# Kernel tuning notes

Hardware: AMD Instinct MI355X
Metric: run time of the kernel (lower is better)

Reference implementation:

```python
import jax, jax.numpy as jnp
import numpy as np

N_NODES = 50000
N_EDGES = 800000
IN_CH = 14     # x has 2 pos cols + 14 feature cols
HID = 16
N_REGIONS = 10


def _init_linear(key, fan_in, fan_out):
    k1, k2 = jax.random.split(key)
    bound = 1.0 / np.sqrt(fan_in)
    W = jax.random.uniform(k1, (fan_in, fan_out), minval=-bound, maxval=bound, dtype=jnp.float32)
    b = jax.random.uniform(k2, (fan_out,), minval=-bound, maxval=bound, dtype=jnp.float32)
    return W, b


def setup_inputs() -> dict:
    key = jax.random.key(0)
    ks = jax.random.split(key, 16)
    x = jax.random.normal(ks[0], (N_NODES, 2 + IN_CH), dtype=jnp.float32)
    edge_index = jax.random.randint(ks[1], (2, N_EDGES), 0, N_NODES, dtype=jnp.int64)
    node_region = jax.random.randint(ks[2], (N_NODES,), 0, N_REGIONS, dtype=jnp.int64)

    inp = {"x": x, "edge_index": edge_index, "node_region": node_region}
    # 3 RSGCN layers: lin_in maps coors(2) -> in_c*hidden, lin_out maps hidden -> hidden
    in_chs = [IN_CH, HID, HID]
    for li, ic in enumerate(in_chs, start=1):
        Wi, bi = _init_linear(ks[2 + 2 * li], 2, ic * HID)
        Wo, bo = _init_linear(ks[3 + 2 * li], HID, HID)
        inp[f"W_in{li}"] = Wi; inp[f"b_in{li}"] = bi
        inp[f"W_out{li}"] = Wo; inp[f"b_out{li}"] = bo
    # decoder
    inp["Wd1"], inp["bd1"] = _init_linear(ks[10], 2 * HID, HID)
    inp["Wd2"], inp["bd2"] = _init_linear(ks[11], HID, HID)
    inp["Wd3"], inp["bd3"] = _init_linear(ks[12], HID, 1)
    return inp


def _rsgcn_layer(h, pos, src, dst, same_region, W_in, b_in, W_out, b_out):
    # Spatial graph conv (SGCN-style) with region-specific gating.
    E = src.shape[0]
    in_c = h.shape[1]
    rel = pos[dst] - pos[src]                                   # [E, 2]
    spatial = jax.nn.relu(rel @ W_in + b_in).reshape(E, in_c, HID)  # [E, in_c, hid]
    msg = jnp.einsum('ec,ech->eh', h[src], spatial)             # [E, hid]
    msg = msg * same_region                                     # region-specific gate
    agg = jax.ops.segment_sum(msg, dst, num_segments=N_NODES)   # [N, hid]
    cnt = jax.ops.segment_sum(jnp.ones((E,), h.dtype), dst, num_segments=N_NODES)
    agg = agg / jnp.maximum(cnt, 1.0)[:, None]                  # mean aggregation
    return jax.nn.relu(agg @ W_out + b_out)                     # dropout is identity in eval


def reference(x, edge_index, node_region,
              W_in1, b_in1, W_out1, b_out1,
              W_in2, b_in2, W_out2, b_out2,
              W_in3, b_in3, W_out3, b_out3,
              Wd1, bd1, Wd2, bd2, Wd3, bd3):
    pos = x[:, :2]
    h = x[:, 2:]
    src, dst = edge_index[0], edge_index[1]
    same = (node_region[src] == node_region[dst]).astype(x.dtype)[:, None]
    h = _rsgcn_layer(h, pos, src, dst, same, W_in1, b_in1, W_out1, b_out1)
    h = _rsgcn_layer(h, pos, src, dst, same, W_in2, b_in2, W_out2, b_out2)
    h = _rsgcn_layer(h, pos, src, dst, same, W_in3, b_in3, W_out3, b_out3)
    # decoder: per-edge link score
    z = jnp.concatenate([h[src], h[dst]], axis=-1)              # [E, 2*hid]
    z = jax.nn.relu(z @ Wd1 + bd1)
    z = jax.nn.relu(z @ Wd2 + bd2)
    return jax.nn.sigmoid(z @ Wd3 + bd3)                        # [E, 1]
```

## Files before the change

### kernel.cpp

```cpp
#include <hip/hip_runtime.h>
#include <math.h>

#define N_NODES 50000
#define N_EDGES 800000
#define HID 16
#define SCAN_BLOCKS ((N_NODES + 255) / 256)

__global__ void count_kernel(const int* __restrict__ src,
                             const int* __restrict__ dst,
                             const int* __restrict__ region,
                             int* __restrict__ cnt_all,
                             int* __restrict__ cnt_act) {
    int e = blockIdx.x * blockDim.x + threadIdx.x;
    int s = src[e];
    int d = dst[e];
    atomicAdd(cnt_all + d, 1);
    if (region[s] == region[d]) atomicAdd(cnt_act + d, 1);
}

__global__ void scanA_kernel(const int* __restrict__ cnt_act,
                             int* __restrict__ blockSums) {
    __shared__ int red[256];
    int i = blockIdx.x * 256 + threadIdx.x;
    red[threadIdx.x] = (i < N_NODES) ? cnt_act[i] : 0;
    __syncthreads();
    for (int off = 128; off > 0; off >>= 1) {
        if (threadIdx.x < off) red[threadIdx.x] += red[threadIdx.x + off];
        __syncthreads();
    }
    if (threadIdx.x == 0) blockSums[blockIdx.x] = red[0];
}

__global__ void scanB_kernel(const int* __restrict__ blockSums,
                             int* __restrict__ blockOff) {
    __shared__ int s[256];
    int t = threadIdx.x;
    s[t] = (t < SCAN_BLOCKS) ? blockSums[t] : 0;
    __syncthreads();
    for (int off = 1; off < 256; off <<= 1) {
        int v = (t >= off) ? s[t - off] : 0;
        __syncthreads();
        s[t] += v;
        __syncthreads();
    }
    if (t < SCAN_BLOCKS) blockOff[t] = (t == 0) ? 0 : s[t - 1];
}

__global__ void scanC_kernel(const int* __restrict__ cnt_act,
                             const int* __restrict__ blockOff,
                             int* __restrict__ row_ptr) {
    __shared__ int s[256];
    int t = threadIdx.x;
    int i = blockIdx.x * 256 + t;
    int v = (i < N_NODES) ? cnt_act[i] : 0;
    s[t] = v;
    __syncthreads();
    for (int off = 1; off < 256; off <<= 1) {
        int u = (t >= off) ? s[t - off] : 0;
        __syncthreads();
        s[t] += u;
        __syncthreads();
    }
    if (i < N_NODES) row_ptr[i] = blockOff[blockIdx.x] + s[t] - v;
}

__global__ void fill_kernel(const int* __restrict__ src,
                            const int* __restrict__ dst,
                            const int* __restrict__ region,
                            const int* __restrict__ row_ptr,
                            int* __restrict__ cursor,
                            int* __restrict__ csr_eid) {
    int e = blockIdx.x * blockDim.x + threadIdx.x;
    int s = src[e];
    int d = dst[e];
    if (region[s] == region[d]) {
        int pos = row_ptr[d] + atomicAdd(cursor + d, 1);
        csr_eid[pos] = e;
    }
}

template <int IN_C>
__global__ void layer_gather(const float* __restrict__ x,
                             const float* __restrict__ hbase,
                             const int* __restrict__ src,
                             const int* __restrict__ csr_eid,
                             const int* __restrict__ row_ptr,
                             const int* __restrict__ cnt_act,
                             const int* __restrict__ cnt_all,
                             const float* __restrict__ Win,
                             const float* __restrict__ bin,
                             const float* __restrict__ Wout,
                             const float* __restrict__ bout,
                             float* __restrict__ hout) {
    int t = blockIdx.x * blockDim.x + threadIdx.x;
    int n = t >> 4;
    int j = t & 15;

    float w0[IN_C], w1[IN_C], bb[IN_C];
#pragma unroll
    for (int c = 0; c < IN_C; ++c) {
        w0[c] = Win[c * HID + j];
        w1[c] = Win[IN_C * HID + c * HID + j];
        bb[c] = bin[c * HID + j];
    }

    float px = x[n * 16 + 0];
    float py = x[n * 16 + 1];

    int beg = row_ptr[n];
    int cntA = cnt_act[n];

    float msg = 0.0f;
    for (int k = 0; k < cntA; ++k) {
        int e = csr_eid[beg + k];
        int s = src[e];
        float rx = px - x[s * 16 + 0];
        float ry = py - x[s * 16 + 1];
        const float* hs = hbase + s * 16;
        float m = 0.0f;
#pragma unroll
        for (int c = 0; c < IN_C; ++c) {
            float sp = fmaf(rx, w0[c], fmaf(ry, w1[c], bb[c]));
            sp = fmaxf(sp, 0.0f);
            m = fmaf(hs[c], sp, m);
        }
        msg += m;
    }

    float inv = 1.0f / fmaxf((float)cnt_all[n], 1.0f);
    float a = msg * inv;

    int lane_base = (threadIdx.x & 63) & 0x30;
    float o = bout[j];
#pragma unroll
    for (int c = 0; c < HID; ++c) {
        float ac = __shfl(a, lane_base + c, 64);
        o = fmaf(ac, Wout[c * HID + j], o);
    }
    hout[n * HID + j] = fmaxf(o, 0.0f);
}

__global__ void decoder_kernel(const float* __restrict__ h,
                               const int* __restrict__ src,
                               const int* __restrict__ dst,
                               const float* __restrict__ Wd1,
                               const float* __restrict__ bd1,
                               const float* __restrict__ Wd2,
                               const float* __restrict__ bd2,
                               const float* __restrict__ Wd3,
                               const float* __restrict__ bd3,
                               float* __restrict__ out) {
    int e = blockIdx.x * blockDim.x + threadIdx.x;
    if (e >= N_EDGES) return;
    int s = src[e];
    int d = dst[e];

    float z[32];
    const float4* hs = (const float4*)(h + s * HID);
    const float4* hd = (const float4*)(h + d * HID);
#pragma unroll
    for (int q = 0; q < 4; ++q) {
        float4 v = hs[q];
        z[q * 4 + 0] = v.x; z[q * 4 + 1] = v.y; z[q * 4 + 2] = v.z; z[q * 4 + 3] = v.w;
    }
#pragma unroll
    for (int q = 0; q < 4; ++q) {
        float4 v = hd[q];
        z[16 + q * 4 + 0] = v.x; z[16 + q * 4 + 1] = v.y; z[16 + q * 4 + 2] = v.z; z[16 + q * 4 + 3] = v.w;
    }

    float d1[HID];
#pragma unroll
    for (int j = 0; j < HID; ++j) d1[j] = bd1[j];
#pragma unroll
    for (int c = 0; c < 32; ++c) {
        float zc = z[c];
#pragma unroll
        for (int j = 0; j < HID; ++j) d1[j] = fmaf(zc, Wd1[c * HID + j], d1[j]);
    }
#pragma unroll
    for (int j = 0; j < HID; ++j) d1[j] = fmaxf(d1[j], 0.0f);

    float d2[HID];
#pragma unroll
    for (int j = 0; j < HID; ++j) d2[j] = bd2[j];
#pragma unroll
    for (int c = 0; c < HID; ++c) {
        float dc = d1[c];
#pragma unroll
        for (int j = 0; j < HID; ++j) d2[j] = fmaf(dc, Wd2[c * HID + j], d2[j]);
    }

    float o = bd3[0];
#pragma unroll
    for (int j = 0; j < HID; ++j) o = fmaf(fmaxf(d2[j], 0.0f), Wd3[j], o);

    out[e] = 1.0f / (1.0f + __expf(-o));
}

extern "C" void kernel_launch(void* const* d_in, const int* in_sizes, int n_in,
                              void* d_out, int out_size, void* d_ws, size_t ws_size,
                              hipStream_t stream) {
    const float* x      = (const float*)d_in[0];
    const int*   edge   = (const int*)d_in[1];
    const int*   region = (const int*)d_in[2];
    const float* W_in1  = (const float*)d_in[3];
    const float* b_in1  = (const float*)d_in[4];
    const float* W_out1 = (const float*)d_in[5];
    const float* b_out1 = (const float*)d_in[6];
    const float* W_in2  = (const float*)d_in[7];
    const float* b_in2  = (const float*)d_in[8];
    const float* W_out2 = (const float*)d_in[9];
    const float* b_out2 = (const float*)d_in[10];
    const float* W_in3  = (const float*)d_in[11];
    const float* b_in3  = (const float*)d_in[12];
    const float* W_out3 = (const float*)d_in[13];
    const float* b_out3 = (const float*)d_in[14];
    const float* Wd1    = (const float*)d_in[15];
    const float* bd1    = (const float*)d_in[16];
    const float* Wd2    = (const float*)d_in[17];
    const float* bd2    = (const float*)d_in[18];
    const float* Wd3    = (const float*)d_in[19];
    const float* bd3    = (const float*)d_in[20];
    float* out = (float*)d_out;

    const int* src = edge;
    const int* dst = edge + N_EDGES;

    float* ws        = (float*)d_ws;
    float* hA        = ws;
    float* hB        = hA + N_NODES * HID;
    int*   cnt_all   = (int*)(hB + N_NODES * HID);
    int*   cnt_act   = cnt_all + N_NODES;
    int*   row_ptr   = cnt_act + N_NODES;
    int*   cursor    = row_ptr + N_NODES;
    int*   blockSums = cursor + N_NODES;
    int*   blockOff  = blockSums + 256;
    int*   csr_eid   = (int*)d_out;

    const int BLK = 256;
    const int egrid = N_EDGES / BLK;
    const int lgrid = N_NODES * HID / BLK;

    hipMemsetAsync(cnt_all, 0, (size_t)(4 * N_NODES) * sizeof(int), stream);

    count_kernel<<<egrid, BLK, 0, stream>>>(src, dst, region, cnt_all, cnt_act);
    scanA_kernel<<<SCAN_BLOCKS, 256, 0, stream>>>(cnt_act, blockSums);
    scanB_kernel<<<1, 256, 0, stream>>>(blockSums, blockOff);
    scanC_kernel<<<SCAN_BLOCKS, 256, 0, stream>>>(cnt_act, blockOff, row_ptr);
    fill_kernel<<<egrid, BLK, 0, stream>>>(src, dst, region, row_ptr, cursor, csr_eid);

    layer_gather<14><<<lgrid, BLK, 0, stream>>>(x, x + 2, src, csr_eid, row_ptr,
                                                cnt_act, cnt_all, W_in1, b_in1,
                                                W_out1, b_out1, hA);
    layer_gather<16><<<lgrid, BLK, 0, stream>>>(x, hA, src, csr_eid, row_ptr,
                                                cnt_act, cnt_all, W_in2, b_in2,
                                                W_out2, b_out2, hB);
    layer_gather<16><<<lgrid, BLK, 0, stream>>>(x, hB, src, csr_eid, row_ptr,
                                                cnt_act, cnt_all, W_in3, b_in3,
                                                W_out3, b_out3, hA);

    decoder_kernel<<<egrid, BLK, 0, stream>>>(hA, src, dst, Wd1, bd1, Wd2, bd2, Wd3, bd3, out);
}
```

Baseline: 242.0 us.

## Precompute per-node decoder first-layer projections and process four edges per thread

The first decoder linear layer is split into per-node halves. The last GCN layer now computes u = h·Wd1_top and v = h·Wd1_bottom once per node, so the per-edge work becomes an add of u[src] and v[dst] instead of a 32x16 matmul. The decoder also handles four edges per thread, using vectorized int4 index loads, shared Wd2 row loads and a float4 output store. This trades a larger per-node buffer (32 floats per node) and higher register pressure for far fewer per-edge FLOPs.

```diff
diff --git a/kernel.cpp b/kernel.cpp
--- a/kernel.cpp
+++ b/kernel.cpp
@@ -5,6 +5,7 @@
 #define N_EDGES 800000
 #define HID 16
 #define SCAN_BLOCKS ((N_NODES + 255) / 256)
+#define EPT 4
 
 __global__ void count_kernel(const int* __restrict__ src,
                              const int* __restrict__ dst,
@@ -79,7 +80,7 @@
     }
 }
 
-template <int IN_C>
+template <int IN_C, bool WRITE_UV>
 __global__ void layer_gather(const float* __restrict__ x,
                              const float* __restrict__ hbase,
                              const int* __restrict__ src,
@@ -91,6 +92,7 @@
                              const float* __restrict__ bin,
                              const float* __restrict__ Wout,
                              const float* __restrict__ bout,
+                             const float* __restrict__ Wd1,
                              float* __restrict__ hout) {
     int t = blockIdx.x * blockDim.x + threadIdx.x;
     int n = t >> 4;
@@ -137,65 +139,115 @@
         float ac = __shfl(a, lane_base + c, 64);
         o = fmaf(ac, Wout[c * HID + j], o);
     }
-    hout[n * HID + j] = fmaxf(o, 0.0f);
-}
-
-__global__ void decoder_kernel(const float* __restrict__ h,
+    float hval = fmaxf(o, 0.0f);
+
+    if (!WRITE_UV) {
+        hout[n * HID + j] = hval;
+    } else {
+        float u = 0.0f, v = 0.0f;
+#pragma unroll
+        for (int c = 0; c < HID; ++c) {
+            float hc = __shfl(hval, lane_base + c, 64);
+            u = fmaf(hc, Wd1[c * HID + j], u);
+            v = fmaf(hc, Wd1[(HID + c) * HID + j], v);
+        }
+        hout[n * 32 + j]       = u;
+        hout[n * 32 + 16 + j]  = v;
+    }
+}
+
+__global__ void decoder_kernel(const float* __restrict__ uv,
                                const int* __restrict__ src,
                                const int* __restrict__ dst,
-                               const float* __restrict__ Wd1,
                                const float* __restrict__ bd1,
                                const float* __restrict__ Wd2,
                                const float* __restrict__ bd2,
                                const float* __restrict__ Wd3,
                                const float* __restrict__ bd3,
                                float* __restrict__ out) {
-    int e = blockIdx.x * blockDim.x + threadIdx.x;
-    if (e >= N_EDGES) return;
-    int s = src[e];
-    int d = dst[e];
-
-    float z[32];
-    const float4* hs = (const float4*)(h + s * HID);
-    const float4* hd = (const float4*)(h + d * HID);
+    int i = blockIdx.x * blockDim.x + threadIdx.x;
+    if (i * EPT >= N_EDGES) return;
+
+    const int4* src4 = (const int4*)src;
+    const int4* dst4 = (const int4*)dst;
+    int4 s4 = src4[i];
+    int4 d4 = dst4[i];
+    int ss[EPT] = {s4.x, s4.y, s4.z, s4.w};
+    int dd[EPT] = {d4.x, d4.y, d4.z, d4.w};
+
+    float b1[HID];
+    const float4* b1p = (const float4*)bd1;
 #pragma unroll
     for (int q = 0; q < 4; ++q) {
-        float4 v = hs[q];
-        z[q * 4 + 0] = v.x; z[q * 4 + 1] = v.y; z[q * 4 + 2] = v.z; z[q * 4 + 3] = v.w;
-    }
+        float4 b = b1p[q];
+        b1[q*4+0] = b.x; b1[q*4+1] = b.y; b1[q*4+2] = b.z; b1[q*4+3] = b.w;
+    }
+
+    float d1[EPT][HID];
+#pragma unroll
+    for (int e = 0; e < EPT; ++e) {
+        const float4* us = (const float4*)(uv + (size_t)ss[e] * 32);
+        const float4* vd = (const float4*)(uv + (size_t)dd[e] * 32 + 16);
+#pragma unroll
+        for (int q = 0; q < 4; ++q) {
+            float4 a = us[q];
+            float4 b = vd[q];
+            d1[e][q*4+0] = fmaxf(a.x + b.x + b1[q*4+0], 0.0f);
+            d1[e][q*4+1] = fmaxf(a.y + b.y + b1[q*4+1], 0.0f);
+            d1[e][q*4+2] = fmaxf(a.z + b.z + b1[q*4+2], 0.0f);
+            d1[e][q*4+3] = fmaxf(a.w + b.w + b1[q*4+3], 0.0f);
+        }
+    }
+
+    float acc[EPT][HID];
+    const float4* b2p = (const float4*)bd2;
 #pragma unroll
     for (int q = 0; q < 4; ++q) {
-        float4 v = hd[q];
-        z[16 + q * 4 + 0] = v.x; z[16 + q * 4 + 1] = v.y; z[16 + q * 4 + 2] = v.z; z[16 + q * 4 + 3] = v.w;
-    }
-
-    float d1[HID];
-#pragma unroll
-    for (int j = 0; j < HID; ++j) d1[j] = bd1[j];
-#pragma unroll
-    for (int c = 0; c < 32; ++c) {
-        float zc = z[c];
-#pragma unroll
-        for (int j = 0; j < HID; ++j) d1[j] = fmaf(zc, Wd1[c * HID + j], d1[j]);
-    }
-#pragma unroll
-    for (int j = 0; j < HID; ++j) d1[j] = fmaxf(d1[j], 0.0f);
-
-    float d2[HID];
-#pragma unroll
-    for (int j = 0; j < HID; ++j) d2[j] = bd2[j];
+        float4 b = b2p[q];
+#pragma unroll
+        for (int e = 0; e < EPT; ++e) {
+            acc[e][q*4+0] = b.x; acc[e][q*4+1] = b.y;
+            acc[e][q*4+2] = b.z; acc[e][q*4+3] = b.w;
+        }
+    }
+
 #pragma unroll
     for (int c = 0; c < HID; ++c) {
-        float dc = d1[c];
-#pragma unroll
-        for (int j = 0; j < HID; ++j) d2[j] = fmaf(dc, Wd2[c * HID + j], d2[j]);
-    }
-
-    float o = bd3[0];
-#pragma unroll
-    for (int j = 0; j < HID; ++j) o = fmaf(fmaxf(d2[j], 0.0f), Wd3[j], o);
-
-    out[e] = 1.0f / (1.0f + __expf(-o));
+        const float4* wr = (const float4*)(Wd2 + c * HID);
+        float w[HID];
+#pragma unroll
+        for (int q = 0; q < 4; ++q) {
+            float4 wv = wr[q];
+            w[q*4+0] = wv.x; w[q*4+1] = wv.y; w[q*4+2] = wv.z; w[q*4+3] = wv.w;
+        }
+#pragma unroll
+        for (int e = 0; e < EPT; ++e) {
+            float dc = d1[e][c];
+#pragma unroll
+            for (int j = 0; j < HID; ++j) acc[e][j] = fmaf(dc, w[j], acc[e][j]);
+        }
+    }
+
+    float w3[HID];
+    const float4* w3p = (const float4*)Wd3;
+#pragma unroll
+    for (int q = 0; q < 4; ++q) {
+        float4 wv = w3p[q];
+        w3[q*4+0] = wv.x; w3[q*4+1] = wv.y; w3[q*4+2] = wv.z; w3[q*4+3] = wv.w;
+    }
+    float b3 = bd3[0];
+
+    float4 res;
+    float r[EPT];
+#pragma unroll
+    for (int e = 0; e < EPT; ++e) {
+        float o = b3;
+#pragma unroll
+        for (int j = 0; j < HID; ++j) o = fmaf(fmaxf(acc[e][j], 0.0f), w3[j], o);
+        r[e] = 1.0f / (1.0f + __expf(-o));
+    }
+    res.x = r[0]; res.y = r[1]; res.z = r[2]; res.w = r[3];
+    ((float4*)out)[i] = res;
 }
 
 extern "C" void kernel_launch(void* const* d_in, const int* in_sizes, int n_in,
@@ -230,7 +282,8 @@
     float* ws        = (float*)d_ws;
     float* hA        = ws;
     float* hB        = hA + N_NODES * HID;
-    int*   cnt_all   = (int*)(hB + N_NODES * HID);
+    float* uv        = hB + N_NODES * HID;
+    int*   cnt_all   = (int*)(uv + N_NODES * 32);
     int*   cnt_act   = cnt_all + N_NODES;
     int*   row_ptr   = cnt_act + N_NODES;
     int*   cursor    = row_ptr + N_NODES;
@@ -241,6 +294,7 @@
     const int BLK = 256;
     const int egrid = N_EDGES / BLK;
     const int lgrid = N_NODES * HID / BLK;
+    const int dgrid = (N_EDGES / EPT + BLK - 1) / BLK;
 
     hipMemsetAsync(cnt_all, 0, (size_t)(4 * N_NODES) * sizeof(int), stream);
 
@@ -250,15 +304,15 @@
     scanC_kernel<<<SCAN_BLOCKS, 256, 0, stream>>>(cnt_act, blockOff, row_ptr);
     fill_kernel<<<egrid, BLK, 0, stream>>>(src, dst, region, row_ptr, cursor, csr_eid);
 
-    layer_gather<14><<<lgrid, BLK, 0, stream>>>(x, x + 2, src, csr_eid, row_ptr,
-                                                cnt_act, cnt_all, W_in1, b_in1,
-                                                W_out1, b_out1, hA);
-    layer_gather<16><<<lgrid, BLK, 0, stream>>>(x, hA, src, csr_eid, row_ptr,
-                                                cnt_act, cnt_all, W_in2, b_in2,
-                                                W_out2, b_out2, hB);
-    layer_gather<16><<<lgrid, BLK, 0, stream>>>(x, hB, src, csr_eid, row_ptr,
-                                                cnt_act, cnt_all, W_in3, b_in3,
-                                                W_out3, b_out3, hA);
-
-    decoder_kernel<<<egrid, BLK, 0, stream>>>(hA, src, dst, Wd1, bd1, Wd2, bd2, Wd3, bd3, out);
-}
+    layer_gather<14, false><<<lgrid, BLK, 0, stream>>>(x, x + 2, src, csr_eid, row_ptr,
+                                                       cnt_act, cnt_all, W_in1, b_in1,
+                                                       W_out1, b_out1, nullptr, hA);
+    layer_gather<16, false><<<lgrid, BLK, 0, stream>>>(x, hA, src, csr_eid, row_ptr,
+                                                       cnt_act, cnt_all, W_in2, b_in2,
+                                                       W_out2, b_out2, nullptr, hB);
+    layer_gather<16, true><<<lgrid, BLK, 0, stream>>>(x, hB, src, csr_eid, row_ptr,
+                                                      cnt_act, cnt_all, W_in3, b_in3,
+                                                      W_out3, b_out3, Wd1, uv);
+
+    decoder_kernel<<<dgrid, BLK, 0, stream>>>(uv, src, dst, bd1, Wd2, bd2, Wd3, bd3, out);
+}
```

New measurement: 257.7 us. 1.07x slower.

## Precompute per-edge CSR records with source id and relative position

Applied to the files above, without the earlier changes.

The fill kernel now writes a packed float4 record per active edge (source index plus precomputed relative position) into CSR order. This removes the csr_eid->src->x indirection chain in all three gather layers. The block-offset scan and row-pointer scan are merged into one kernel that also seeds the cursor and computes inverse degree, which drops a kernel launch and a memset region. The decoder is reordered to use fewer live registers. The cost is extra workspace for the records and extra writes in the fill pass.

```diff
diff --git a/kernel.cpp b/kernel.cpp
--- a/kernel.cpp
+++ b/kernel.cpp
@@ -5,13 +5,14 @@
 #define N_EDGES 800000
 #define HID 16
 #define SCAN_BLOCKS ((N_NODES + 255) / 256)
+#define BLK 256
 
 __global__ void count_kernel(const int* __restrict__ src,
                              const int* __restrict__ dst,
                              const int* __restrict__ region,
                              int* __restrict__ cnt_all,
                              int* __restrict__ cnt_act) {
-    int e = blockIdx.x * blockDim.x + threadIdx.x;
+    int e = blockIdx.x * BLK + threadIdx.x;
     int s = src[e];
     int d = dst[e];
     atomicAdd(cnt_all + d, 1);
@@ -20,79 +21,90 @@
 
 __global__ void scanA_kernel(const int* __restrict__ cnt_act,
                              int* __restrict__ blockSums) {
-    __shared__ int red[256];
+    __shared__ int lds[256];
     int i = blockIdx.x * 256 + threadIdx.x;
-    red[threadIdx.x] = (i < N_NODES) ? cnt_act[i] : 0;
+    lds[threadIdx.x] = (i < N_NODES) ? cnt_act[i] : 0;
     __syncthreads();
     for (int off = 128; off > 0; off >>= 1) {
-        if (threadIdx.x < off) red[threadIdx.x] += red[threadIdx.x + off];
-        __syncthreads();
-    }
-    if (threadIdx.x == 0) blockSums[blockIdx.x] = red[0];
-}
-
-__global__ void scanB_kernel(const int* __restrict__ blockSums,
-                             int* __restrict__ blockOff) {
-    __shared__ int s[256];
+        if (threadIdx.x < off) lds[threadIdx.x] += lds[threadIdx.x + off];
+        __syncthreads();
+    }
+    if (threadIdx.x == 0) blockSums[blockIdx.x] = lds[0];
+}
+
+__global__ void scanBC_kernel(const int* __restrict__ cnt_act,
+                              const int* __restrict__ cnt_all,
+                              const int* __restrict__ blockSums,
+                              int* __restrict__ row_ptr,
+                              int* __restrict__ cursor,
+                              float* __restrict__ invDeg) {
+    __shared__ int ldsA[256];
+    __shared__ int ldsB[256];
     int t = threadIdx.x;
-    s[t] = (t < SCAN_BLOCKS) ? blockSums[t] : 0;
+    ldsB[t] = (t < SCAN_BLOCKS) ? blockSums[t] : 0;
     __syncthreads();
     for (int off = 1; off < 256; off <<= 1) {
-        int v = (t >= off) ? s[t - off] : 0;
-        __syncthreads();
-        s[t] += v;
-        __syncthreads();
-    }
-    if (t < SCAN_BLOCKS) blockOff[t] = (t == 0) ? 0 : s[t - 1];
-}
-
-__global__ void scanC_kernel(const int* __restrict__ cnt_act,
-                             const int* __restrict__ blockOff,
-                             int* __restrict__ row_ptr) {
-    __shared__ int s[256];
-    int t = threadIdx.x;
+        int u = (t >= off) ? ldsB[t - off] : 0;
+        __syncthreads();
+        ldsB[t] += u;
+        __syncthreads();
+    }
+    int blockOff = (blockIdx.x == 0) ? 0 : ldsB[blockIdx.x - 1];
+
     int i = blockIdx.x * 256 + t;
     int v = (i < N_NODES) ? cnt_act[i] : 0;
-    s[t] = v;
+    ldsA[t] = v;
     __syncthreads();
     for (int off = 1; off < 256; off <<= 1) {
-        int u = (t >= off) ? s[t - off] : 0;
-        __syncthreads();
-        s[t] += u;
-        __syncthreads();
-    }
-    if (i < N_NODES) row_ptr[i] = blockOff[blockIdx.x] + s[t] - v;
+        int u = (t >= off) ? ldsA[t - off] : 0;
+        __syncthreads();
+        ldsA[t] += u;
+        __syncthreads();
+    }
+    if (i < N_NODES) {
+        int rp = blockOff + ldsA[t] - v;
+        row_ptr[i] = rp;
+        cursor[i]  = rp;
+        invDeg[i]  = 1.0f / fmaxf((float)cnt_all[i], 1.0f);
+    }
 }
 
 __global__ void fill_kernel(const int* __restrict__ src,
                             const int* __restrict__ dst,
                             const int* __restrict__ region,
-                            const int* __restrict__ row_ptr,
+                            const float* __restrict__ x,
                             int* __restrict__ cursor,
-                            int* __restrict__ csr_eid) {
-    int e = blockIdx.x * blockDim.x + threadIdx.x;
+                            float4* __restrict__ recs) {
+    int e = blockIdx.x * BLK + threadIdx.x;
     int s = src[e];
     int d = dst[e];
     if (region[s] == region[d]) {
-        int pos = row_ptr[d] + atomicAdd(cursor + d, 1);
-        csr_eid[pos] = e;
+        int pos = atomicAdd(cursor + d, 1);
+        const float2* pd = (const float2*)(x + (size_t)d * 16);
+        const float2* ps = (const float2*)(x + (size_t)s * 16);
+        float2 xd = *pd;
+        float2 xs = *ps;
+        float4 rec;
+        rec.x = __int_as_float(s);
+        rec.y = xd.x - xs.x;
+        rec.z = xd.y - xs.y;
+        rec.w = 0.0f;
+        recs[pos] = rec;
     }
 }
 
 template <int IN_C>
-__global__ void layer_gather(const float* __restrict__ x,
-                             const float* __restrict__ hbase,
-                             const int* __restrict__ src,
-                             const int* __restrict__ csr_eid,
-                             const int* __restrict__ row_ptr,
-                             const int* __restrict__ cnt_act,
-                             const int* __restrict__ cnt_all,
-                             const float* __restrict__ Win,
-                             const float* __restrict__ bin,
-                             const float* __restrict__ Wout,
-                             const float* __restrict__ bout,
-                             float* __restrict__ hout) {
-    int t = blockIdx.x * blockDim.x + threadIdx.x;
+__global__ void gather_kernel(const float* __restrict__ hbase,
+                              const float4* __restrict__ recs,
+                              const int* __restrict__ row_ptr,
+                              const int* __restrict__ cnt_act,
+                              const float* __restrict__ invDeg,
+                              const float* __restrict__ Win,
+                              const float* __restrict__ bin,
+                              const float* __restrict__ Wout,
+                              const float* __restrict__ bout,
+                              float* __restrict__ hout) {
+    int t = blockIdx.x * BLK + threadIdx.x;
     int n = t >> 4;
     int j = t & 15;
 
@@ -104,19 +116,16 @@
         bb[c] = bin[c * HID + j];
     }
 
-    float px = x[n * 16 + 0];
-    float py = x[n * 16 + 1];
-
-    int beg = row_ptr[n];
+    int beg  = row_ptr[n];
     int cntA = cnt_act[n];
 
     float msg = 0.0f;
     for (int k = 0; k < cntA; ++k) {
-        int e = csr_eid[beg + k];
-        int s = src[e];
-        float rx = px - x[s * 16 + 0];
-        float ry = py - x[s * 16 + 1];
-        const float* hs = hbase + s * 16;
+        float4 rec = recs[beg + k];
+        int   s  = __float_as_int(rec.x);
+        float rx = rec.y;
+        float ry = rec.z;
+        const float* hs = hbase + (size_t)s * 16;
         float m = 0.0f;
 #pragma unroll
         for (int c = 0; c < IN_C; ++c) {
@@ -127,8 +136,7 @@
         msg += m;
     }
 
-    float inv = 1.0f / fmaxf((float)cnt_all[n], 1.0f);
-    float a = msg * inv;
+    float a = msg * invDeg[n];
 
     int lane_base = (threadIdx.x & 63) & 0x30;
     float o = bout[j];
@@ -150,33 +158,38 @@
                                const float* __restrict__ Wd3,
                                const float* __restrict__ bd3,
                                float* __restrict__ out) {
-    int e = blockIdx.x * blockDim.x + threadIdx.x;
-    if (e >= N_EDGES) return;
+    int e = blockIdx.x * BLK + threadIdx.x;
     int s = src[e];
     int d = dst[e];
 
-    float z[32];
-    const float4* hs = (const float4*)(h + s * HID);
-    const float4* hd = (const float4*)(h + d * HID);
+    float hv[HID];
+    float d1[HID];
+#pragma unroll
+    for (int j = 0; j < HID; ++j) d1[j] = bd1[j];
+
+    const float4* h4 = (const float4*)(h + (size_t)s * HID);
 #pragma unroll
     for (int q = 0; q < 4; ++q) {
-        float4 v = hs[q];
-        z[q * 4 + 0] = v.x; z[q * 4 + 1] = v.y; z[q * 4 + 2] = v.z; z[q * 4 + 3] = v.w;
-    }
+        float4 v = h4[q];
+        hv[q*4+0] = v.x; hv[q*4+1] = v.y; hv[q*4+2] = v.z; hv[q*4+3] = v.w;
+    }
+#pragma unroll
+    for (int c = 0; c < HID; ++c) {
+        float hc = hv[c];
+#pragma unroll
+        for (int j = 0; j < HID; ++j) d1[j] = fmaf(hc, Wd1[c * HID + j], d1[j]);
+    }
+    h4 = (const float4*)(h + (size_t)d * HID);
 #pragma unroll
     for (int q = 0; q < 4; ++q) {
-        float4 v = hd[q];
-        z[16 + q * 4 + 0] = v.x; z[16 + q * 4 + 1] = v.y; z[16 + q * 4 + 2] = v.z; z[16 + q * 4 + 3] = v.w;
-    }
-
-    float d1[HID];
-#pragma unroll
-    for (int j = 0; j < HID; ++j) d1[j] = bd1[j];
-#pragma unroll
-    for (int c = 0; c < 32; ++c) {
-        float zc = z[c];
-#pragma unroll
-        for (int j = 0; j < HID; ++j) d1[j] = fmaf(zc, Wd1[c * HID + j], d1[j]);
+        float4 v = h4[q];
+        hv[q*4+0] = v.x; hv[q*4+1] = v.y; hv[q*4+2] = v.z; hv[q*4+3] = v.w;
+    }
+#pragma unroll
+    for (int c = 0; c < HID; ++c) {
+        float hc = hv[c];
+#pragma unroll
+        for (int j = 0; j < HID; ++j) d1[j] = fmaf(hc, Wd1[(HID + c) * HID + j], d1[j]);
     }
 #pragma unroll
     for (int j = 0; j < HID; ++j) d1[j] = fmaxf(d1[j], 0.0f);
@@ -235,30 +248,26 @@
     int*   row_ptr   = cnt_act + N_NODES;
     int*   cursor    = row_ptr + N_NODES;
     int*   blockSums = cursor + N_NODES;
-    int*   blockOff  = blockSums + 256;
-    int*   csr_eid   = (int*)d_out;
-
-    const int BLK = 256;
+    float* invDeg    = (float*)(blockSums + 256);
+    float4* recs     = (float4*)(invDeg + N_NODES);
+
     const int egrid = N_EDGES / BLK;
     const int lgrid = N_NODES * HID / BLK;
 
-    hipMemsetAsync(cnt_all, 0, (size_t)(4 * N_NODES) * sizeof(int), stream);
+    hipMemsetAsync(cnt_all, 0, (size_t)(2 * N_NODES) * sizeof(int), stream);
 
     count_kernel<<<egrid, BLK, 0, stream>>>(src, dst, region, cnt_all, cnt_act);
     scanA_kernel<<<SCAN_BLOCKS, 256, 0, stream>>>(cnt_act, blockSums);
-    scanB_kernel<<<1, 256, 0, stream>>>(blockSums, blockOff);
-    scanC_kernel<<<SCAN_BLOCKS, 256, 0, stream>>>(cnt_act, blockOff, row_ptr);
-    fill_kernel<<<egrid, BLK, 0, stream>>>(src, dst, region, row_ptr, cursor, csr_eid);
-
-    layer_gather<14><<<lgrid, BLK, 0, stream>>>(x, x + 2, src, csr_eid, row_ptr,
-                                                cnt_act, cnt_all, W_in1, b_in1,
-                                                W_out1, b_out1, hA);
-    layer_gather<16><<<lgrid, BLK, 0, stream>>>(x, hA, src, csr_eid, row_ptr,
-                                                cnt_act, cnt_all, W_in2, b_in2,
-                                                W_out2, b_out2, hB);
-    layer_gather<16><<<lgrid, BLK, 0, stream>>>(x, hB, src, csr_eid, row_ptr,
-                                                cnt_act, cnt_all, W_in3, b_in3,
-                                                W_out3, b_out3, hA);
+    scanBC_kernel<<<SCAN_BLOCKS, 256, 0, stream>>>(cnt_act, cnt_all, blockSums,
+                                                   row_ptr, cursor, invDeg);
+    fill_kernel<<<egrid, BLK, 0, stream>>>(src, dst, region, x, cursor, recs);
+
+    gather_kernel<14><<<lgrid, BLK, 0, stream>>>(x + 2, recs, row_ptr, cnt_act, invDeg,
+                                                 W_in1, b_in1, W_out1, b_out1, hA);
+    gather_kernel<16><<<lgrid, BLK, 0, stream>>>(hA, recs, row_ptr, cnt_act, invDeg,
+                                                 W_in2, b_in2, W_out2, b_out2, hB);
+    gather_kernel<16><<<lgrid, BLK, 0, stream>>>(hB, recs, row_ptr, cnt_act, invDeg,
+                                                 W_in3, b_in3, W_out3, b_out3, hA);
 
     decoder_kernel<<<egrid, BLK, 0, stream>>>(hA, src, dst, Wd1, bd1, Wd2, bd2, Wd3, bd3, out);
 }
```

Measured after the change: 233.6 us. 3.5% less time.
